# Optimization experiments

Measured on AMD Instinct MI355X. Metric: run time of the kernel, lower is better.

The kernel has to match this reference:

```python
import jax, jax.numpy as jnp
import numpy as np

N_NODES = 100000
N_EDGES = 1600000
IN_DIM = 64
HID_DIM = 128
OUT_DIM = 128


def setup_inputs() -> dict:
    key = jax.random.key(0)
    ks = jax.random.split(key, 12)
    s = 0.05
    return {
        "x": jax.random.normal(ks[0], (N_NODES, IN_DIM), jnp.float32),
        "edge_index": jax.random.randint(ks[1], (2, N_EDGES), 0, N_NODES, jnp.int64),
        "edge_attr": jax.random.uniform(ks[2], (N_EDGES, 2), jnp.float32),
        # conv1 MLP: Linear(IN+2, HID) -> ReLU -> Linear(HID, HID)
        "W11": jax.random.normal(ks[3], (IN_DIM + 2, HID_DIM), jnp.float32) * s,
        "b11": jax.random.normal(ks[4], (HID_DIM,), jnp.float32) * s,
        "W12": jax.random.normal(ks[5], (HID_DIM, HID_DIM), jnp.float32) * s,
        "b12": jax.random.normal(ks[6], (HID_DIM,), jnp.float32) * s,
        # conv2 MLP: Linear(HID+2, OUT) -> ReLU -> Linear(OUT, OUT)
        "W21": jax.random.normal(ks[7], (HID_DIM + 2, OUT_DIM), jnp.float32) * s,
        "b21": jax.random.normal(ks[8], (OUT_DIM,), jnp.float32) * s,
        "W22": jax.random.normal(ks[9], (OUT_DIM, OUT_DIM), jnp.float32) * s,
        "b22": jax.random.normal(ks[10], (OUT_DIM,), jnp.float32) * s,
    }


def _gin_conv(x, edge_index, edge_attr, W1, b1, W2, b2):
    N = x.shape[0]
    loop = jnp.arange(N, dtype=edge_index.dtype)
    src = jnp.concatenate([edge_index[0], loop])  # [E+N] message sources
    dst = jnp.concatenate([edge_index[1], loop])  # [E+N] aggregation targets
    # self-loop edge_attr filled with 1.0 (PyG add_self_loops default)
    ea = jnp.concatenate([edge_attr, jnp.ones((N, edge_attr.shape[1]), edge_attr.dtype)], axis=0)
    m = jnp.concatenate([x[src], ea], axis=-1)  # [E+N, F+2] gather + concat
    h = jnp.dot(jax.nn.relu(jnp.dot(m, W1) + b1), W2) + b2  # edge MLP
    return jax.ops.segment_sum(h, dst, num_segments=N)  # scatter-add aggregate


def reference(x, edge_index, edge_attr, W11, b11, W12, b12, W21, b21, W22, b22):
    h = _gin_conv(x, edge_index, edge_attr, W11, b11, W12, b12)
    h = jax.nn.relu(h)
    return _gin_conv(h, edge_index, edge_attr, W21, b21, W22, b22)
```

## Files before the change

### kernel.cpp

```cpp
#include <hip/hip_runtime.h>


typedef unsigned int uint;
typedef __attribute__((ext_vector_type(8))) short bf16x8;
typedef __attribute__((ext_vector_type(4))) float f32x4;

#define BSHIFT 9
#define BNODES (1 << BSHIFT)

static __device__ __forceinline__ unsigned short f2bf(float f) {
    uint u = __float_as_uint(f);
    uint r = (u + 0x7fffu + ((u >> 16) & 1u)) >> 16;
    return (unsigned short)r;
}


__global__ void wprep_all(const float* __restrict__ W11, const float* __restrict__ W12,
                          const float* __restrict__ W21, const float* __restrict__ W22,
                          unsigned short* Wt11, unsigned short* Wt12,
                          unsigned short* Wt21, unsigned short* Wt22,
                          int* bcnt, int* ptr, int N, int E) {
    int idx = blockIdx.x * 256 + threadIdx.x;
    if (idx < 256) bcnt[idx] = 0;
    if (idx == 0) ptr[N] = E;
    const float* W; unsigned short* Wt; int K; int off;
    if (idx < 64 * 128)        { W = W11; Wt = Wt11; K = 64;  off = idx; }
    else if (idx < 192 * 128)  { W = W12; Wt = Wt12; K = 128; off = idx - 64 * 128; }
    else if (idx < 320 * 128)  { W = W21; Wt = Wt21; K = 128; off = idx - 192 * 128; }
    else if (idx < 448 * 128)  { W = W22; Wt = Wt22; K = 128; off = idx - 320 * 128; }
    else return;
    int k = off >> 7, n = off & 127;
    Wt[n * K + k] = f2bf(W[k * 128 + n]);
}


__global__ __launch_bounds__(512) void bin_kernel(
    const int* __restrict__ src, const int* __restrict__ dst,
    const float* __restrict__ ea, int* __restrict__ bcnt,
    int2* __restrict__ barr, int CAP, int E, int B) {
    __shared__ int hist[256];
    __shared__ int bbase[256];
    __shared__ int gbase[256];
    __shared__ int wtot[4];
    __shared__ int2 sorted[4096];
    __shared__ unsigned char bof[4096];
    const int tileBase = blockIdx.x * 4096;
    int n = E - tileBase; if (n > 4096) n = 4096; if (n <= 0) return;
    const int tid = threadIdx.x;
    const int lane = tid & 63;
    if (tid < 256) hist[tid] = 0;
    __syncthreads();

    int2 ent[8]; int bk[8]; int rk[8];
#pragma unroll
    for (int kk = 0; kk < 8; kk++) {
        int i = kk * 512 + tid;
        bk[kk] = -1;
        if (i < n) {
            int e = tileBase + i;
            int s = src[e], d = dst[e];
            float2 a = reinterpret_cast<const float2*>(ea)[e];
            int b = d >> BSHIFT;
            int dloc = d & (BNODES - 1);
            ent[kk].x = s | (dloc << 17);
            ent[kk].y = (int)((uint)f2bf(a.x) | ((uint)f2bf(a.y) << 16));
            bk[kk] = b;
            rk[kk] = atomicAdd(&hist[b], 1);
        }
    }
    __syncthreads();
    int hv = (tid < 256) ? hist[tid] : 0;
    int inc = hv;
#pragma unroll
    for (int off = 1; off < 64; off <<= 1) {
        int tt = __shfl_up(inc, off, 64);
        if (lane >= off) inc += tt;
    }
    if ((tid >> 6) < 4 && lane == 63) wtot[tid >> 6] = inc;
    __syncthreads();
    if (tid == 0) { int run = 0; for (int i = 0; i < 4; i++) { int tt = wtot[i]; wtot[i] = run; run += tt; } }
    __syncthreads();
    if (tid < 256) bbase[tid] = inc - hv + wtot[tid >> 6];
    if (tid < B && hist[tid] > 0) gbase[tid] = atomicAdd(&bcnt[tid], hist[tid]);
    __syncthreads();
#pragma unroll
    for (int kk = 0; kk < 8; kk++) {
        if (bk[kk] >= 0) {
            int p = bbase[bk[kk]] + rk[kk];
            sorted[p] = ent[kk];
            bof[p] = (unsigned char)bk[kk];
        }
    }
    __syncthreads();
    for (int i = tid; i < n; i += 512) {
        int b = bof[i];
        barr[(long)b * CAP + gbase[b] + (i - bbase[b])] = sorted[i];
    }
}


static __device__ void csr_body(const int2* __restrict__ barr, const int* __restrict__ bcnt,
                                int CAP, int N, int2* __restrict__ csr, int* __restrict__ ptr) {
    __shared__ int hist[BNODES];
    __shared__ int lptr[BNODES];
    __shared__ int wtot[8];
    __shared__ int sbase;
    const int g = blockIdx.x;
    const int tid = threadIdx.x;
    const int lane = tid & 63;
    const int cnt = bcnt[g];
    if (tid == 0) sbase = 0;
    hist[tid] = 0;
    __syncthreads();
    if (tid < g) atomicAdd(&sbase, bcnt[tid]);
    const int2* my = barr + (long)g * CAP;
    for (int i = tid; i < cnt; i += 512)
        atomicAdd(&hist[((uint)my[i].x) >> 17], 1);
    __syncthreads();
    int v = hist[tid];
    int inc = v;
#pragma unroll
    for (int off = 1; off < 64; off <<= 1) {
        int tt = __shfl_up(inc, off, 64);
        if (lane >= off) inc += tt;
    }
    if (lane == 63) wtot[tid >> 6] = inc;
    __syncthreads();
    if (tid == 0) { int run = 0; for (int i = 0; i < 8; i++) { int tt = wtot[i]; wtot[i] = run; run += tt; } }
    __syncthreads();
    const int base = sbase;
    int excl = inc - v + wtot[tid >> 6];
    lptr[tid] = excl;
    int gnode = g * BNODES + tid;
    if (gnode < N) ptr[gnode] = base + excl;
    __syncthreads();
    for (int i = tid; i < cnt; i += 512) {
        int2 e = my[i];
        int pos = base + atomicAdd(&lptr[((uint)e.x) >> 17], 1);
        int2 o; o.x = e.x & 0x1FFFF; o.y = e.y;
        csr[pos] = o;
    }
}


template <int K, bool IN_F32, bool OUT_BF16, bool USE_CNT, bool RELU>
static __device__ __forceinline__ void gemm_body(
    const void* __restrict__ Ain, const unsigned short* __restrict__ Wt,
    const float* __restrict__ bias, const int* __restrict__ ptr,
    void* __restrict__ Cout, int N, int tid, long rowBase) {
    constexpr int KS = K / 32;
    const int wave = tid >> 6;
    const int lane = tid & 63;
    const int m = lane & 15, quad = lane >> 4;

    bf16x8 bfrag[2][KS];
#pragma unroll
    for (int ct = 0; ct < 2; ct++) {
        int col = (wave * 2 + ct) * 16 + m;
#pragma unroll
        for (int ks = 0; ks < KS; ks++)
            bfrag[ct][ks] = *(const bf16x8*)(Wt + (long)col * K + ks * 32 + quad * 8);
    }

#pragma unroll
    for (int rt = 0; rt < 4; rt++) {
        long row = rowBase + rt * 16 + m;
        long rc = row < N ? row : (long)N - 1;
        bf16x8 afrag[KS];
        if (IN_F32) {
            const float* arow = (const float*)Ain + rc * K;
#pragma unroll
            for (int ks = 0; ks < KS; ks++) {
                float4 lo = *(const float4*)(arow + ks * 32 + quad * 8);
                float4 hi = *(const float4*)(arow + ks * 32 + quad * 8 + 4);
                bf16x8 f;
                f[0] = (short)f2bf(lo.x); f[1] = (short)f2bf(lo.y);
                f[2] = (short)f2bf(lo.z); f[3] = (short)f2bf(lo.w);
                f[4] = (short)f2bf(hi.x); f[5] = (short)f2bf(hi.y);
                f[6] = (short)f2bf(hi.z); f[7] = (short)f2bf(hi.w);
                afrag[ks] = f;
            }
        } else {
            const unsigned short* arow = (const unsigned short*)Ain + rc * K;
#pragma unroll
            for (int ks = 0; ks < KS; ks++)
                afrag[ks] = *(const bf16x8*)(arow + ks * 32 + quad * 8);
        }

#pragma unroll
        for (int ct = 0; ct < 2; ct++) {
            f32x4 acc = {0.f, 0.f, 0.f, 0.f};
#pragma unroll
            for (int ks = 0; ks < KS; ks++)
                acc = __builtin_amdgcn_mfma_f32_16x16x32_bf16(afrag[ks], bfrag[ct][ks], acc, 0, 0, 0);

            int col = (wave * 2 + ct) * 16 + m;
            float b = bias[col];
#pragma unroll
            for (int r = 0; r < 4; r++) {
                long orow = rowBase + rt * 16 + quad * 4 + r;
                if (orow < N) {
                    float v = acc[r];
                    if (USE_CNT) v += b * (float)(ptr[orow + 1] - ptr[orow] + 1);
                    else v += b;
                    if (RELU) v = fmaxf(v, 0.f);
                    if (OUT_BF16) ((unsigned short*)Cout)[orow * 128 + col] = f2bf(v);
                    else ((float*)Cout)[orow * 128 + col] = v;
                }
            }
        }
    }
}

template <int K, bool IN_F32, bool OUT_BF16, bool USE_CNT, bool RELU>
__global__ __launch_bounds__(256) void gemm_mfma(
    const void* __restrict__ Ain, const unsigned short* __restrict__ Wt,
    const float* __restrict__ bias, const int* __restrict__ ptr,
    void* __restrict__ Cout, int N) {
    gemm_body<K, IN_F32, OUT_BF16, USE_CNT, RELU>(Ain, Wt, bias, ptr, Cout, N,
                                                  threadIdx.x, (long)blockIdx.x * 64);
}


__global__ __launch_bounds__(512) void csr_gemm1(
    const int2* __restrict__ barr, const int* __restrict__ bcnt, int CAP, int N,
    int2* __restrict__ csr, int* __restrict__ ptr, int CSRB,
    const float* __restrict__ x, const unsigned short* __restrict__ Wt11,
    const float* __restrict__ b11, unsigned short* __restrict__ A_bf) {
    if ((int)blockIdx.x < CSRB) {
        csr_body(barr, bcnt, CAP, N, csr, ptr);
    } else {
        int bid = blockIdx.x - CSRB;
        int sub = threadIdx.x >> 8;
        gemm_body<64, true, true, false, false>(x, Wt11, b11, nullptr, A_bf, N,
                                                threadIdx.x & 255,
                                                (long)bid * 128 + sub * 64);
    }
}


__global__ __launch_bounds__(256) void gather_kernel(
    const uint* __restrict__ Au, const int* __restrict__ ptr,
    const int2* __restrict__ csr, const float* __restrict__ we,
    uint* __restrict__ Bout, int N) {
    int node = blockIdx.x * 4 + (threadIdx.x >> 6);
    if (node >= N) return;
    node = __builtin_amdgcn_readfirstlane(node);
    const int t = threadIdx.x & 63;
    const int c = 2 * t;
    const float w0x = we[c], w0y = we[c + 1];
    const float w1x = we[128 + c], w1y = we[128 + c + 1];

    const char* Ab = (const char*)Au;
    const uint t4 = (uint)t * 4u;
#define LD(sidx) (*(const uint*)(Ab + ((((uint)(sidx)) << 8) + t4)))
#define ACC(rv, ev)                                                      \
    {                                                                    \
        float a0 = __uint_as_float(((uint)(ev)) << 16);                  \
        float a1 = __uint_as_float(((uint)(ev)) & 0xffff0000u);          \
        float vx = __uint_as_float((rv) << 16);                          \
        float vy = __uint_as_float((rv) & 0xffff0000u);                  \
        vx = fmaf(a0, w0x, fmaf(a1, w1x, vx));                           \
        vy = fmaf(a0, w0y, fmaf(a1, w1y, vy));                           \
        ax += fmaxf(vx, 0.f);                                            \
        ay += fmaxf(vy, 0.f);                                            \
    }
#define EDGE(i, off)                                                     \
    int2 c##i = csr[k + (off)];                                          \
    uint s##i = (uint)__builtin_amdgcn_readfirstlane(c##i.x);            \
    uint e##i = (uint)__builtin_amdgcn_readfirstlane(c##i.y);

    uint selfv = LD((uint)node);
    float ax = fmaxf(__uint_as_float(selfv << 16) + w0x + w1x, 0.f);
    float ay = fmaxf(__uint_as_float(selfv & 0xffff0000u) + w0y + w1y, 0.f);

    int k   = __builtin_amdgcn_readfirstlane(ptr[node]);
    int end = __builtin_amdgcn_readfirstlane(ptr[node + 1]);

    for (; k + 8 <= end; k += 8) {
        EDGE(0, 0) EDGE(1, 1) EDGE(2, 2) EDGE(3, 3)
        EDGE(4, 4) EDGE(5, 5) EDGE(6, 6) EDGE(7, 7)
        uint r0 = LD(s0); uint r1 = LD(s1); uint r2 = LD(s2); uint r3 = LD(s3);
        uint r4 = LD(s4); uint r5 = LD(s5); uint r6 = LD(s6); uint r7 = LD(s7);
        ACC(r0, e0) ACC(r1, e1) ACC(r2, e2) ACC(r3, e3)
        ACC(r4, e4) ACC(r5, e5) ACC(r6, e6) ACC(r7, e7)
    }
    for (; k + 4 <= end; k += 4) {
        EDGE(0, 0) EDGE(1, 1) EDGE(2, 2) EDGE(3, 3)
        uint r0 = LD(s0); uint r1 = LD(s1); uint r2 = LD(s2); uint r3 = LD(s3);
        ACC(r0, e0) ACC(r1, e1) ACC(r2, e2) ACC(r3, e3)
    }
    for (; k < end; k++) {
        EDGE(0, 0)
        uint r0 = LD(s0);
        ACC(r0, e0)
    }
#undef EDGE
#undef ACC
#undef LD
    uint outv = (uint)f2bf(ax) | ((uint)f2bf(ay) << 16);
    __builtin_nontemporal_store(outv, Bout + (long)node * 64 + t);
}


__global__ __launch_bounds__(256) void fused_mid_gemm(
    const unsigned short* __restrict__ Bin, const int* __restrict__ ptr,
    const unsigned short* __restrict__ WtA, const float* __restrict__ biasA,
    const unsigned short* __restrict__ WtB, const float* __restrict__ biasB,
    unsigned short* __restrict__ Cout, int N) {
    __shared__ unsigned short ts[64 * 136];
    const int wave = threadIdx.x >> 6;
    const int lane = threadIdx.x & 63;
    const int m = lane & 15, quad = lane >> 4;
    const long rowBase = (long)blockIdx.x * 64;

    bf16x8 bfrag[2][4];
#pragma unroll
    for (int ct = 0; ct < 2; ct++) {
        int col = (wave * 2 + ct) * 16 + m;
#pragma unroll
        for (int ks = 0; ks < 4; ks++)
            bfrag[ct][ks] = *(const bf16x8*)(WtA + (long)col * 128 + ks * 32 + quad * 8);
    }

    f32x4 acc[4][2];
#pragma unroll
    for (int rt = 0; rt < 4; rt++) {
        long row = rowBase + rt * 16 + m;
        long rc = row < N ? row : (long)N - 1;
        const unsigned short* arow = Bin + rc * 128;
        bf16x8 af[4];
#pragma unroll
        for (int ks = 0; ks < 4; ks++)
            af[ks] = *(const bf16x8*)(arow + ks * 32 + quad * 8);
#pragma unroll
        for (int ct = 0; ct < 2; ct++) {
            f32x4 a = {0.f, 0.f, 0.f, 0.f};
#pragma unroll
            for (int ks = 0; ks < 4; ks++)
                a = __builtin_amdgcn_mfma_f32_16x16x32_bf16(af[ks], bfrag[ct][ks], a, 0, 0, 0);
            acc[rt][ct] = a;
        }
    }

#pragma unroll
    for (int rt = 0; rt < 4; rt++) {
        float cntf[4];
#pragma unroll
        for (int r = 0; r < 4; r++) {
            long grow = rowBase + rt * 16 + quad * 4 + r;
            cntf[r] = (grow < N) ? (float)(ptr[grow + 1] - ptr[grow] + 1) : 1.f;
        }
#pragma unroll
        for (int ct = 0; ct < 2; ct++) {
            int col = (wave * 2 + ct) * 16 + m;
            float b = biasA[col];
#pragma unroll
            for (int r = 0; r < 4; r++) {
                int row = rt * 16 + quad * 4 + r;
                ts[row * 136 + col] = f2bf(fmaxf(acc[rt][ct][r] + b * cntf[r], 0.f));
            }
        }
    }
    __syncthreads();

#pragma unroll
    for (int ct = 0; ct < 2; ct++) {
        int col = (wave * 2 + ct) * 16 + m;
#pragma unroll
        for (int ks = 0; ks < 4; ks++)
            bfrag[ct][ks] = *(const bf16x8*)(WtB + (long)col * 128 + ks * 32 + quad * 8);
    }
#pragma unroll
    for (int rt = 0; rt < 4; rt++) {
        const unsigned short* lr = ts + (rt * 16 + m) * 136;
        bf16x8 af[4];
#pragma unroll
        for (int ks = 0; ks < 4; ks++)
            af[ks] = *(const bf16x8*)(lr + ks * 32 + quad * 8);
#pragma unroll
        for (int ct = 0; ct < 2; ct++) {
            f32x4 a = {0.f, 0.f, 0.f, 0.f};
#pragma unroll
            for (int ks = 0; ks < 4; ks++)
                a = __builtin_amdgcn_mfma_f32_16x16x32_bf16(af[ks], bfrag[ct][ks], a, 0, 0, 0);
            int col = (wave * 2 + ct) * 16 + m;
            float b = biasB[col];
#pragma unroll
            for (int r = 0; r < 4; r++) {
                long grow = rowBase + rt * 16 + quad * 4 + r;
                if (grow < N) Cout[grow * 128 + col] = f2bf(a[r] + b);
            }
        }
    }
}


extern "C" void kernel_launch(void* const* d_in, const int* in_sizes, int n_in,
                              void* d_out, int out_size, void* d_ws, size_t ws_size,
                              hipStream_t stream) {
    const float* x   = (const float*)d_in[0];
    const int*   ei  = (const int*)d_in[1];
    const float* ea  = (const float*)d_in[2];
    const float* W11 = (const float*)d_in[3];
    const float* b11 = (const float*)d_in[4];
    const float* W12 = (const float*)d_in[5];
    const float* b12 = (const float*)d_in[6];
    const float* W21 = (const float*)d_in[7];
    const float* b21 = (const float*)d_in[8];
    const float* W22 = (const float*)d_in[9];
    const float* b22 = (const float*)d_in[10];
    float* out = (float*)d_out;

    const int N = in_sizes[0] / 64;
    const int E = in_sizes[1] / 2;
    const int* src = ei;
    const int* dst = ei + E;

    const int B = (N + BNODES - 1) >> BSHIFT;
    const int CAP = E / B + 4096;

    char* p = (char*)d_ws;
    unsigned short* A_bf = (unsigned short*)p;  p += (size_t)N * 128 * 2;
    unsigned short* B_bf = (unsigned short*)p;
    int2* barr = (int2*)B_bf;                   p += (size_t)N * 128 * 2;
    int2* csr  = (int2*)p;                      p += (size_t)E * 8;
    int* ptr   = (int*)p;                       p += (size_t)(N + 1) * 4;
    int* bcnt  = (int*)p;                       p += 256 * 4;
    unsigned short* Wt11 = (unsigned short*)p;  p += (size_t)64 * 128 * 2;
    unsigned short* Wt12 = (unsigned short*)p;  p += (size_t)128 * 128 * 2;
    unsigned short* Wt21 = (unsigned short*)p;  p += (size_t)128 * 128 * 2;
    unsigned short* Wt22 = (unsigned short*)p;

    const int binBlocks = (E + 4095) / 4096;
    const int gatherBlocks = (N + 3) / 4;
    const int tileBlocks = (N + 63) / 64;
    const int g1Tiles = (N + 127) / 128;

    wprep_all<<<224, 256, 0, stream>>>(W11, W12, W21, W22,
                                       Wt11, Wt12, Wt21, Wt22,
                                       bcnt, ptr, N, E);
    bin_kernel<<<binBlocks, 512, 0, stream>>>(src, dst, ea, bcnt, barr, CAP, E, B);
    csr_gemm1<<<B + g1Tiles, 512, 0, stream>>>(barr, bcnt, CAP, N, csr, ptr, B,
                                               x, Wt11, b11, A_bf);
    gather_kernel<<<gatherBlocks, 256, 0, stream>>>((const uint*)A_bf, ptr, csr,
                                                    W11 + 64 * 128, (uint*)B_bf, N);
    fused_mid_gemm<<<tileBlocks, 256, 0, stream>>>(B_bf, ptr, Wt12, b12, Wt21, b21, A_bf, N);
    gather_kernel<<<gatherBlocks, 256, 0, stream>>>((const uint*)A_bf, ptr, csr,
                                                    W21 + 128 * 128, (uint*)B_bf, N);
    gemm_mfma<128, false, false, true, false><<<tileBlocks, 256, 0, stream>>>(
        B_bf, Wt22, b22, ptr, out, N);
}
```

Baseline: 364.0 us.

## Fuse edge gather into following MFMA GEMMs via shared-memory tiles

The per-node gather/aggregate is now done inside the GEMM kernels: each 256-thread block gathers 64 nodes (16 per wave) into an LDS tile, then runs the MFMA GEMMs on that tile. This removes the global write and re-read of the intermediate bf16 aggregated features and two kernel launches, and ping-pongs between two workspace buffers. In exchange, each wave handles 16 nodes sequentially instead of one, which cuts memory-level parallelism and exposes load imbalance in the latency-bound gather. The gather blocks are also 16x fewer, and GEMM work is serialized behind the gather in each block.

New measurement: 347.3 us. 1.05x faster.

```diff
diff --git a/kernel.cpp b/kernel.cpp
--- a/kernel.cpp
+++ b/kernel.cpp
@@ -212,15 +212,6 @@
     }
 }
 
-template <int K, bool IN_F32, bool OUT_BF16, bool USE_CNT, bool RELU>
-__global__ __launch_bounds__(256) void gemm_mfma(
-    const void* __restrict__ Ain, const unsigned short* __restrict__ Wt,
-    const float* __restrict__ bias, const int* __restrict__ ptr,
-    void* __restrict__ Cout, int N) {
-    gemm_body<K, IN_F32, OUT_BF16, USE_CNT, RELU>(Ain, Wt, bias, ptr, Cout, N,
-                                                  threadIdx.x, (long)blockIdx.x * 64);
-}
-
 
 __global__ __launch_bounds__(512) void csr_gemm1(
     const int2* __restrict__ barr, const int* __restrict__ bcnt, int CAP, int N,
@@ -239,18 +230,15 @@
 }
 
 
-__global__ __launch_bounds__(256) void gather_kernel(
+static __device__ __forceinline__ void gather_lds(
     const uint* __restrict__ Au, const int* __restrict__ ptr,
     const int2* __restrict__ csr, const float* __restrict__ we,
-    uint* __restrict__ Bout, int N) {
-    int node = blockIdx.x * 4 + (threadIdx.x >> 6);
-    if (node >= N) return;
-    node = __builtin_amdgcn_readfirstlane(node);
-    const int t = threadIdx.x & 63;
+    uint* __restrict__ ts_u, int N, int tid, int rowBase) {
+    const int w = tid >> 6;
+    const int t = tid & 63;
     const int c = 2 * t;
     const float w0x = we[c], w0y = we[c + 1];
     const float w1x = we[128 + c], w1y = we[128 + c + 1];
-
     const char* Ab = (const char*)Au;
     const uint t4 = (uint)t * 4u;
 #define LD(sidx) (*(const uint*)(Ab + ((((uint)(sidx)) << 8) + t4)))
@@ -270,49 +258,59 @@
     uint s##i = (uint)__builtin_amdgcn_readfirstlane(c##i.x);            \
     uint e##i = (uint)__builtin_amdgcn_readfirstlane(c##i.y);
 
-    uint selfv = LD((uint)node);
-    float ax = fmaxf(__uint_as_float(selfv << 16) + w0x + w1x, 0.f);
-    float ay = fmaxf(__uint_as_float(selfv & 0xffff0000u) + w0y + w1y, 0.f);
-
-    int k   = __builtin_amdgcn_readfirstlane(ptr[node]);
-    int end = __builtin_amdgcn_readfirstlane(ptr[node + 1]);
-
-    for (; k + 8 <= end; k += 8) {
-        EDGE(0, 0) EDGE(1, 1) EDGE(2, 2) EDGE(3, 3)
-        EDGE(4, 4) EDGE(5, 5) EDGE(6, 6) EDGE(7, 7)
-        uint r0 = LD(s0); uint r1 = LD(s1); uint r2 = LD(s2); uint r3 = LD(s3);
-        uint r4 = LD(s4); uint r5 = LD(s5); uint r6 = LD(s6); uint r7 = LD(s7);
-        ACC(r0, e0) ACC(r1, e1) ACC(r2, e2) ACC(r3, e3)
-        ACC(r4, e4) ACC(r5, e5) ACC(r6, e6) ACC(r7, e7)
-    }
-    for (; k + 4 <= end; k += 4) {
-        EDGE(0, 0) EDGE(1, 1) EDGE(2, 2) EDGE(3, 3)
-        uint r0 = LD(s0); uint r1 = LD(s1); uint r2 = LD(s2); uint r3 = LD(s3);
-        ACC(r0, e0) ACC(r1, e1) ACC(r2, e2) ACC(r3, e3)
-    }
-    for (; k < end; k++) {
-        EDGE(0, 0)
-        uint r0 = LD(s0);
-        ACC(r0, e0)
+    for (int i = 0; i < 16; i++) {
+        int node = rowBase + w * 16 + i;
+        if (node >= N) break;
+
+        uint selfv = LD((uint)node);
+        float ax = fmaxf(__uint_as_float(selfv << 16) + w0x + w1x, 0.f);
+        float ay = fmaxf(__uint_as_float(selfv & 0xffff0000u) + w0y + w1y, 0.f);
+
+        int k   = __builtin_amdgcn_readfirstlane(ptr[node]);
+        int end = __builtin_amdgcn_readfirstlane(ptr[node + 1]);
+
+        for (; k + 8 <= end; k += 8) {
+            EDGE(0, 0) EDGE(1, 1) EDGE(2, 2) EDGE(3, 3)
+            EDGE(4, 4) EDGE(5, 5) EDGE(6, 6) EDGE(7, 7)
+            uint r0 = LD(s0); uint r1 = LD(s1); uint r2 = LD(s2); uint r3 = LD(s3);
+            uint r4 = LD(s4); uint r5 = LD(s5); uint r6 = LD(s6); uint r7 = LD(s7);
+            ACC(r0, e0) ACC(r1, e1) ACC(r2, e2) ACC(r3, e3)
+            ACC(r4, e4) ACC(r5, e5) ACC(r6, e6) ACC(r7, e7)
+        }
+        for (; k + 4 <= end; k += 4) {
+            EDGE(0, 0) EDGE(1, 1) EDGE(2, 2) EDGE(3, 3)
+            uint r0 = LD(s0); uint r1 = LD(s1); uint r2 = LD(s2); uint r3 = LD(s3);
+            ACC(r0, e0) ACC(r1, e1) ACC(r2, e2) ACC(r3, e3)
+        }
+        for (; k < end; k++) {
+            EDGE(0, 0)
+            uint r0 = LD(s0);
+            ACC(r0, e0)
+        }
+        ts_u[(w * 16 + i) * 68 + t] = (uint)f2bf(ax) | ((uint)f2bf(ay) << 16);
     }
 #undef EDGE
 #undef ACC
 #undef LD
-    uint outv = (uint)f2bf(ax) | ((uint)f2bf(ay) << 16);
-    __builtin_nontemporal_store(outv, Bout + (long)node * 64 + t);
-}
-
-
-__global__ __launch_bounds__(256) void fused_mid_gemm(
-    const unsigned short* __restrict__ Bin, const int* __restrict__ ptr,
+}
+
+
+__global__ __launch_bounds__(256, 4) void gather_mid(
+    const uint* __restrict__ Au, const int* __restrict__ ptr,
+    const int2* __restrict__ csr, const float* __restrict__ we,
     const unsigned short* __restrict__ WtA, const float* __restrict__ biasA,
     const unsigned short* __restrict__ WtB, const float* __restrict__ biasB,
     unsigned short* __restrict__ Cout, int N) {
-    __shared__ unsigned short ts[64 * 136];
-    const int wave = threadIdx.x >> 6;
-    const int lane = threadIdx.x & 63;
+    __shared__ uint ts_u[64 * 68];
+    unsigned short* ts = (unsigned short*)ts_u;
+    const int tid = threadIdx.x;
+    const int rowBase = blockIdx.x * 64;
+
+    gather_lds(Au, ptr, csr, we, ts_u, N, tid, rowBase);
+    __syncthreads();
+
+    const int wave = tid >> 6, lane = tid & 63;
     const int m = lane & 15, quad = lane >> 4;
-    const long rowBase = (long)blockIdx.x * 64;
 
     bf16x8 bfrag[2][4];
 #pragma unroll
@@ -326,13 +324,11 @@
     f32x4 acc[4][2];
 #pragma unroll
     for (int rt = 0; rt < 4; rt++) {
-        long row = rowBase + rt * 16 + m;
-        long rc = row < N ? row : (long)N - 1;
-        const unsigned short* arow = Bin + rc * 128;
+        const unsigned short* lr = ts + (rt * 16 + m) * 136;
         bf16x8 af[4];
 #pragma unroll
         for (int ks = 0; ks < 4; ks++)
-            af[ks] = *(const bf16x8*)(arow + ks * 32 + quad * 8);
+            af[ks] = *(const bf16x8*)(lr + ks * 32 + quad * 8);
 #pragma unroll
         for (int ct = 0; ct < 2; ct++) {
             f32x4 a = {0.f, 0.f, 0.f, 0.f};
@@ -342,6 +338,7 @@
             acc[rt][ct] = a;
         }
     }
+    __syncthreads();
 
 #pragma unroll
     for (int rt = 0; rt < 4; rt++) {
@@ -390,6 +387,59 @@
             for (int r = 0; r < 4; r++) {
                 long grow = rowBase + rt * 16 + quad * 4 + r;
                 if (grow < N) Cout[grow * 128 + col] = f2bf(a[r] + b);
+            }
+        }
+    }
+}
+
+
+__global__ __launch_bounds__(256, 4) void gather_out(
+    const uint* __restrict__ Au, const int* __restrict__ ptr,
+    const int2* __restrict__ csr, const float* __restrict__ we,
+    const unsigned short* __restrict__ Wt, const float* __restrict__ bias,
+    float* __restrict__ out, int N) {
+    __shared__ uint ts_u[64 * 68];
+    unsigned short* ts = (unsigned short*)ts_u;
+    const int tid = threadIdx.x;
+    const int rowBase = blockIdx.x * 64;
+
+    gather_lds(Au, ptr, csr, we, ts_u, N, tid, rowBase);
+    __syncthreads();
+
+    const int wave = tid >> 6, lane = tid & 63;
+    const int m = lane & 15, quad = lane >> 4;
+
+    bf16x8 bfrag[2][4];
+#pragma unroll
+    for (int ct = 0; ct < 2; ct++) {
+        int col = (wave * 2 + ct) * 16 + m;
+#pragma unroll
+        for (int ks = 0; ks < 4; ks++)
+            bfrag[ct][ks] = *(const bf16x8*)(Wt + (long)col * 128 + ks * 32 + quad * 8);
+    }
+
+#pragma unroll
+    for (int rt = 0; rt < 4; rt++) {
+        const unsigned short* lr = ts + (rt * 16 + m) * 136;
+        bf16x8 af[4];
+#pragma unroll
+        for (int ks = 0; ks < 4; ks++)
+            af[ks] = *(const bf16x8*)(lr + ks * 32 + quad * 8);
+#pragma unroll
+        for (int ct = 0; ct < 2; ct++) {
+            f32x4 a = {0.f, 0.f, 0.f, 0.f};
+#pragma unroll
+            for (int ks = 0; ks < 4; ks++)
+                a = __builtin_amdgcn_mfma_f32_16x16x32_bf16(af[ks], bfrag[ct][ks], a, 0, 0, 0);
+            int col = (wave * 2 + ct) * 16 + m;
+            float b = bias[col];
+#pragma unroll
+            for (int r = 0; r < 4; r++) {
+                long grow = rowBase + rt * 16 + quad * 4 + r;
+                if (grow < N) {
+                    float cnt = (float)(ptr[grow + 1] - ptr[grow] + 1);
+                    out[grow * 128 + col] = a[r] + b * cnt;
+                }
             }
         }
     }
@@ -422,8 +472,8 @@
 
     char* p = (char*)d_ws;
     unsigned short* A_bf = (unsigned short*)p;  p += (size_t)N * 128 * 2;
-    unsigned short* B_bf = (unsigned short*)p;
-    int2* barr = (int2*)B_bf;                   p += (size_t)N * 128 * 2;
+    unsigned short* A2_bf = (unsigned short*)p;
+    int2* barr = (int2*)A2_bf;                  p += (size_t)N * 128 * 2;
     int2* csr  = (int2*)p;                      p += (size_t)E * 8;
     int* ptr   = (int*)p;                       p += (size_t)(N + 1) * 4;
     int* bcnt  = (int*)p;                       p += 256 * 4;
@@ -433,7 +483,6 @@
     unsigned short* Wt22 = (unsigned short*)p;
 
     const int binBlocks = (E + 4095) / 4096;
-    const int gatherBlocks = (N + 3) / 4;
     const int tileBlocks = (N + 63) / 64;
     const int g1Tiles = (N + 127) / 128;
 
@@ -443,11 +492,9 @@
     bin_kernel<<<binBlocks, 512, 0, stream>>>(src, dst, ea, bcnt, barr, CAP, E, B);
     csr_gemm1<<<B + g1Tiles, 512, 0, stream>>>(barr, bcnt, CAP, N, csr, ptr, B,
                                                x, Wt11, b11, A_bf);
-    gather_kernel<<<gatherBlocks, 256, 0, stream>>>((const uint*)A_bf, ptr, csr,
-                                                    W11 + 64 * 128, (uint*)B_bf, N);
-    fused_mid_gemm<<<tileBlocks, 256, 0, stream>>>(B_bf, ptr, Wt12, b12, Wt21, b21, A_bf, N);
-    gather_kernel<<<gatherBlocks, 256, 0, stream>>>((const uint*)A_bf, ptr, csr,
-                                                    W21 + 128 * 128, (uint*)B_bf, N);
-    gemm_mfma<128, false, false, true, false><<<tileBlocks, 256, 0, stream>>>(
-        B_bf, Wt22, b22, ptr, out, N);
-}
+    gather_mid<<<tileBlocks, 256, 0, stream>>>((const uint*)A_bf, ptr, csr,
+                                               W11 + 64 * 128, Wt12, b12, Wt21, b21,
+                                               A2_bf, N);
+    gather_out<<<tileBlocks, 256, 0, stream>>>((const uint*)A2_bf, ptr, csr,
+                                               W21 + 128 * 128, Wt22, b22, out, N);
+}
```

## Replace two-level bucket sort with atomic histogram, scan, and atomic scatter CSR build

Applied to the files above, without the earlier changes.

Drops the two-pass bucketed CSR construction, which used a shared-memory local sort followed by a per-bucket counting sort. In its place it runs a global atomic degree histogram, a two-kernel prefix scan, and a direct atomic scatter of edges into CSR slots. The aim is to avoid the intermediate bucket array and the extra passes over it. The cost is heavily contended global atomics, a random-write scatter, two extra launches, and a nondeterministic edge order within each row. The gather tail loop is also reduced from a 4-edge to a 2-edge unroll.

Measured after the change: 487.7 us. 1.34x slower.

```diff
diff --git a/kernel.cpp b/kernel.cpp
--- a/kernel.cpp
+++ b/kernel.cpp
@@ -4,9 +4,6 @@
 typedef unsigned int uint;
 typedef __attribute__((ext_vector_type(8))) short bf16x8;
 typedef __attribute__((ext_vector_type(4))) float f32x4;
-
-#define BSHIFT 9
-#define BNODES (1 << BSHIFT)
 
 static __device__ __forceinline__ unsigned short f2bf(float f) {
     uint u = __float_as_uint(f);
@@ -19,9 +16,9 @@
                           const float* __restrict__ W21, const float* __restrict__ W22,
                           unsigned short* Wt11, unsigned short* Wt12,
                           unsigned short* Wt21, unsigned short* Wt22,
-                          int* bcnt, int* ptr, int N, int E) {
+                          int* cnt, int* ptr, int N, int E) {
     int idx = blockIdx.x * 256 + threadIdx.x;
-    if (idx < 256) bcnt[idx] = 0;
+    if (idx < N) cnt[idx] = 0;
     if (idx == 0) ptr[N] = E;
     const float* W; unsigned short* Wt; int K; int off;
     if (idx < 64 * 128)        { W = W11; Wt = Wt11; K = 64;  off = idx; }
@@ -34,111 +31,59 @@
 }
 
 
-__global__ __launch_bounds__(512) void bin_kernel(
-    const int* __restrict__ src, const int* __restrict__ dst,
-    const float* __restrict__ ea, int* __restrict__ bcnt,
-    int2* __restrict__ barr, int CAP, int E, int B) {
-    __shared__ int hist[256];
-    __shared__ int bbase[256];
-    __shared__ int gbase[256];
-    __shared__ int wtot[4];
-    __shared__ int2 sorted[4096];
-    __shared__ unsigned char bof[4096];
-    const int tileBase = blockIdx.x * 4096;
-    int n = E - tileBase; if (n > 4096) n = 4096; if (n <= 0) return;
+__global__ __launch_bounds__(512) void hist_kernel(
+    const int* __restrict__ dst, int* __restrict__ cnt, int E) {
+    const int base = blockIdx.x * 4096 + threadIdx.x;
+#pragma unroll
+    for (int k = 0; k < 8; k++) {
+        int i = base + k * 512;
+        if (i < E) atomicAdd(&cnt[dst[i]], 1);
+    }
+}
+
+
+__global__ __launch_bounds__(1024) void scanA(
+    int* __restrict__ cnt, int* __restrict__ bsum, int N) {
+    __shared__ int wt[16];
     const int tid = threadIdx.x;
-    const int lane = tid & 63;
-    if (tid < 256) hist[tid] = 0;
+    const int lane = tid & 63, wid = tid >> 6;
+    const int i = blockIdx.x * 1024 + tid;
+    int v = (i < N) ? cnt[i] : 0;
+    int inc = v;
+#pragma unroll
+    for (int off = 1; off < 64; off <<= 1) {
+        int t = __shfl_up(inc, off, 64);
+        if (lane >= off) inc += t;
+    }
+    if (lane == 63) wt[wid] = inc;
     __syncthreads();
-
-    int2 ent[8]; int bk[8]; int rk[8];
-#pragma unroll
-    for (int kk = 0; kk < 8; kk++) {
-        int i = kk * 512 + tid;
-        bk[kk] = -1;
-        if (i < n) {
-            int e = tileBase + i;
-            int s = src[e], d = dst[e];
-            float2 a = reinterpret_cast<const float2*>(ea)[e];
-            int b = d >> BSHIFT;
-            int dloc = d & (BNODES - 1);
-            ent[kk].x = s | (dloc << 17);
-            ent[kk].y = (int)((uint)f2bf(a.x) | ((uint)f2bf(a.y) << 16));
-            bk[kk] = b;
-            rk[kk] = atomicAdd(&hist[b], 1);
-        }
-    }
+    int add = 0;
+#pragma unroll
+    for (int j = 0; j < 16; j++) add += (j < wid) ? wt[j] : 0;
+    if (i < N) cnt[i] = inc - v + add;
+    if (tid == 1023) bsum[blockIdx.x] = add + inc;
+}
+
+
+__global__ __launch_bounds__(1024) void scanC(
+    const int* __restrict__ cnt, const int* __restrict__ bsum,
+    int* __restrict__ ptr, int* __restrict__ ptrw, int N, int NB) {
+    __shared__ int sb[128];
+    __shared__ int bb;
+    const int tid = threadIdx.x;
+    if (tid < 128) sb[tid] = (tid < NB) ? bsum[tid] : 0;
     __syncthreads();
-    int hv = (tid < 256) ? hist[tid] : 0;
-    int inc = hv;
-#pragma unroll
-    for (int off = 1; off < 64; off <<= 1) {
-        int tt = __shfl_up(inc, off, 64);
-        if (lane >= off) inc += tt;
-    }
-    if ((tid >> 6) < 4 && lane == 63) wtot[tid >> 6] = inc;
+    if (tid == 0) {
+        int run = 0;
+        for (int j = 0; j < (int)blockIdx.x; j++) run += sb[j];
+        bb = run;
+    }
     __syncthreads();
-    if (tid == 0) { int run = 0; for (int i = 0; i < 4; i++) { int tt = wtot[i]; wtot[i] = run; run += tt; } }
-    __syncthreads();
-    if (tid < 256) bbase[tid] = inc - hv + wtot[tid >> 6];
-    if (tid < B && hist[tid] > 0) gbase[tid] = atomicAdd(&bcnt[tid], hist[tid]);
-    __syncthreads();
-#pragma unroll
-    for (int kk = 0; kk < 8; kk++) {
-        if (bk[kk] >= 0) {
-            int p = bbase[bk[kk]] + rk[kk];
-            sorted[p] = ent[kk];
-            bof[p] = (unsigned char)bk[kk];
-        }
-    }
-    __syncthreads();
-    for (int i = tid; i < n; i += 512) {
-        int b = bof[i];
-        barr[(long)b * CAP + gbase[b] + (i - bbase[b])] = sorted[i];
-    }
-}
-
-
-static __device__ void csr_body(const int2* __restrict__ barr, const int* __restrict__ bcnt,
-                                int CAP, int N, int2* __restrict__ csr, int* __restrict__ ptr) {
-    __shared__ int hist[BNODES];
-    __shared__ int lptr[BNODES];
-    __shared__ int wtot[8];
-    __shared__ int sbase;
-    const int g = blockIdx.x;
-    const int tid = threadIdx.x;
-    const int lane = tid & 63;
-    const int cnt = bcnt[g];
-    if (tid == 0) sbase = 0;
-    hist[tid] = 0;
-    __syncthreads();
-    if (tid < g) atomicAdd(&sbase, bcnt[tid]);
-    const int2* my = barr + (long)g * CAP;
-    for (int i = tid; i < cnt; i += 512)
-        atomicAdd(&hist[((uint)my[i].x) >> 17], 1);
-    __syncthreads();
-    int v = hist[tid];
-    int inc = v;
-#pragma unroll
-    for (int off = 1; off < 64; off <<= 1) {
-        int tt = __shfl_up(inc, off, 64);
-        if (lane >= off) inc += tt;
-    }
-    if (lane == 63) wtot[tid >> 6] = inc;
-    __syncthreads();
-    if (tid == 0) { int run = 0; for (int i = 0; i < 8; i++) { int tt = wtot[i]; wtot[i] = run; run += tt; } }
-    __syncthreads();
-    const int base = sbase;
-    int excl = inc - v + wtot[tid >> 6];
-    lptr[tid] = excl;
-    int gnode = g * BNODES + tid;
-    if (gnode < N) ptr[gnode] = base + excl;
-    __syncthreads();
-    for (int i = tid; i < cnt; i += 512) {
-        int2 e = my[i];
-        int pos = base + atomicAdd(&lptr[((uint)e.x) >> 17], 1);
-        int2 o; o.x = e.x & 0x1FFFF; o.y = e.y;
-        csr[pos] = o;
+    const int i = blockIdx.x * 1024 + tid;
+    if (i < N) {
+        int p = cnt[i] + bb;
+        ptr[i] = p;
+        ptrw[i] = p;
     }
 }
 
@@ -212,25 +157,30 @@
     }
 }
 
-template <int K, bool IN_F32, bool OUT_BF16, bool USE_CNT, bool RELU>
-__global__ __launch_bounds__(256) void gemm_mfma(
-    const void* __restrict__ Ain, const unsigned short* __restrict__ Wt,
-    const float* __restrict__ bias, const int* __restrict__ ptr,
-    void* __restrict__ Cout, int N) {
-    gemm_body<K, IN_F32, OUT_BF16, USE_CNT, RELU>(Ain, Wt, bias, ptr, Cout, N,
-                                                  threadIdx.x, (long)blockIdx.x * 64);
-}
-
-
-__global__ __launch_bounds__(512) void csr_gemm1(
-    const int2* __restrict__ barr, const int* __restrict__ bcnt, int CAP, int N,
-    int2* __restrict__ csr, int* __restrict__ ptr, int CSRB,
+
+__global__ __launch_bounds__(512) void scatter_gemm1(
+    const int* __restrict__ src, const int* __restrict__ dst,
+    const float* __restrict__ ea, int* __restrict__ ptrw,
+    int2* __restrict__ csr, int SB, int E,
     const float* __restrict__ x, const unsigned short* __restrict__ Wt11,
-    const float* __restrict__ b11, unsigned short* __restrict__ A_bf) {
-    if ((int)blockIdx.x < CSRB) {
-        csr_body(barr, bcnt, CAP, N, csr, ptr);
+    const float* __restrict__ b11, unsigned short* __restrict__ A_bf, int N) {
+    if ((int)blockIdx.x < SB) {
+        const int base = blockIdx.x * 4096 + threadIdx.x;
+#pragma unroll
+        for (int k = 0; k < 8; k++) {
+            int i = base + k * 512;
+            if (i < E) {
+                int s = src[i], d = dst[i];
+                float2 a = reinterpret_cast<const float2*>(ea)[i];
+                int pos = atomicAdd(&ptrw[d], 1);
+                int2 o;
+                o.x = s;
+                o.y = (int)((uint)f2bf(a.x) | ((uint)f2bf(a.y) << 16));
+                csr[pos] = o;
+            }
+        }
     } else {
-        int bid = blockIdx.x - CSRB;
+        int bid = blockIdx.x - SB;
         int sub = threadIdx.x >> 8;
         gemm_body<64, true, true, false, false>(x, Wt11, b11, nullptr, A_bf, N,
                                                 threadIdx.x & 255,
@@ -285,12 +235,12 @@
         ACC(r0, e0) ACC(r1, e1) ACC(r2, e2) ACC(r3, e3)
         ACC(r4, e4) ACC(r5, e5) ACC(r6, e6) ACC(r7, e7)
     }
-    for (; k + 4 <= end; k += 4) {
-        EDGE(0, 0) EDGE(1, 1) EDGE(2, 2) EDGE(3, 3)
-        uint r0 = LD(s0); uint r1 = LD(s1); uint r2 = LD(s2); uint r3 = LD(s3);
-        ACC(r0, e0) ACC(r1, e1) ACC(r2, e2) ACC(r3, e3)
-    }
-    for (; k < end; k++) {
+    for (; k + 2 <= end; k += 2) {
+        EDGE(0, 0) EDGE(1, 1)
+        uint r0 = LD(s0); uint r1 = LD(s1);
+        ACC(r0, e0) ACC(r1, e1)
+    }
+    if (k < end) {
         EDGE(0, 0)
         uint r0 = LD(s0);
         ACC(r0, e0)
@@ -393,6 +343,16 @@
             }
         }
     }
+}
+
+
+template <int K, bool IN_F32, bool OUT_BF16, bool USE_CNT, bool RELU>
+__global__ __launch_bounds__(256) void gemm_mfma(
+    const void* __restrict__ Ain, const unsigned short* __restrict__ Wt,
+    const float* __restrict__ bias, const int* __restrict__ ptr,
+    void* __restrict__ Cout, int N) {
+    gemm_body<K, IN_F32, OUT_BF16, USE_CNT, RELU>(Ain, Wt, bias, ptr, Cout, N,
+                                                  threadIdx.x, (long)blockIdx.x * 64);
 }
 
 
@@ -417,32 +377,34 @@
     const int* src = ei;
     const int* dst = ei + E;
 
-    const int B = (N + BNODES - 1) >> BSHIFT;
-    const int CAP = E / B + 4096;
-
     char* p = (char*)d_ws;
     unsigned short* A_bf = (unsigned short*)p;  p += (size_t)N * 128 * 2;
-    unsigned short* B_bf = (unsigned short*)p;
-    int2* barr = (int2*)B_bf;                   p += (size_t)N * 128 * 2;
+    unsigned short* B_bf = (unsigned short*)p;  p += (size_t)N * 128 * 2;
     int2* csr  = (int2*)p;                      p += (size_t)E * 8;
     int* ptr   = (int*)p;                       p += (size_t)(N + 1) * 4;
-    int* bcnt  = (int*)p;                       p += 256 * 4;
+    int* ptrw  = (int*)p;                       p += (size_t)N * 4;
+    int* cnt   = (int*)p;                       p += (size_t)N * 4;
+    int* bsum  = (int*)p;                       p += 128 * 4;
     unsigned short* Wt11 = (unsigned short*)p;  p += (size_t)64 * 128 * 2;
     unsigned short* Wt12 = (unsigned short*)p;  p += (size_t)128 * 128 * 2;
     unsigned short* Wt21 = (unsigned short*)p;  p += (size_t)128 * 128 * 2;
     unsigned short* Wt22 = (unsigned short*)p;
 
-    const int binBlocks = (E + 4095) / 4096;
+    const int SB = (E + 4095) / 4096;
+    const int NB = (N + 1023) / 1024;
+    const int wprepBlocks = ((N > 448 * 128 ? N : 448 * 128) + 255) / 256;
     const int gatherBlocks = (N + 3) / 4;
     const int tileBlocks = (N + 63) / 64;
     const int g1Tiles = (N + 127) / 128;
 
-    wprep_all<<<224, 256, 0, stream>>>(W11, W12, W21, W22,
-                                       Wt11, Wt12, Wt21, Wt22,
-                                       bcnt, ptr, N, E);
-    bin_kernel<<<binBlocks, 512, 0, stream>>>(src, dst, ea, bcnt, barr, CAP, E, B);
-    csr_gemm1<<<B + g1Tiles, 512, 0, stream>>>(barr, bcnt, CAP, N, csr, ptr, B,
-                                               x, Wt11, b11, A_bf);
+    wprep_all<<<wprepBlocks, 256, 0, stream>>>(W11, W12, W21, W22,
+                                               Wt11, Wt12, Wt21, Wt22,
+                                               cnt, ptr, N, E);
+    hist_kernel<<<SB, 512, 0, stream>>>(dst, cnt, E);
+    scanA<<<NB, 1024, 0, stream>>>(cnt, bsum, N);
+    scanC<<<NB, 1024, 0, stream>>>(cnt, bsum, ptr, ptrw, N, NB);
+    scatter_gemm1<<<SB + g1Tiles, 512, 0, stream>>>(src, dst, ea, ptrw, csr, SB, E,
+                                                    x, Wt11, b11, A_bf, N);
     gather_kernel<<<gatherBlocks, 256, 0, stream>>>((const uint*)A_bf, ptr, csr,
                                                     W11 + 64 * 128, (uint*)B_bf, N);
     fused_mid_gemm<<<tileBlocks, 256, 0, stream>>>(B_bf, ptr, Wt12, b12, Wt21, b21, A_bf, N);
```
